# Optimization experiments

Measured on AMD Instinct MI355X. Metric: run time of the kernel, lower is better.

The kernel has to match this reference:

```python
import jax, jax.numpy as jnp
import numpy as np

LEVEL = 2
INV_SQRT2 = 0.7071067811865476
# subband order: index 0 is the approx (x_coeff1[0]); the 7 details match the
# {'aad','ada','add','daa','dad','dda','ddd'} dict keys of wavedec3 level-`LEVEL`.
SUBS = ['aaa', 'aad', 'ada', 'add', 'daa', 'dad', 'dda', 'ddd']


def dwt1(x, axis):
    # single-level Haar (db1, periodic) analysis along one axis
    x = jnp.moveaxis(x, axis, -1)
    n = x.shape[-1]
    x = x.reshape(*x.shape[:-1], n // 2, 2)
    a = (x[..., 0] + x[..., 1]) * INV_SQRT2
    d = (x[..., 0] - x[..., 1]) * INV_SQRT2
    return jnp.moveaxis(a, -1, axis), jnp.moveaxis(d, -1, axis)


def dwt3(x):
    # separable 3D Haar DWT over the last 3 axes -> 8 subbands keyed 'aaa'..'ddd'
    subs = {'': x}
    for axis in (-3, -2, -1):
        nxt = {}
        for k, v in subs.items():
            a, d = dwt1(v, axis)
            nxt[k + 'a'] = a
            nxt[k + 'd'] = d
        subs = nxt
    return subs


def idwt1(a, d, axis):
    a = jnp.moveaxis(a, axis, -1)
    d = jnp.moveaxis(d, axis, -1)
    x = jnp.stack([(a + d) * INV_SQRT2, (a - d) * INV_SQRT2], axis=-1)
    x = x.reshape(*x.shape[:-2], x.shape[-2] * 2)
    return jnp.moveaxis(x, -1, axis)


def idwt3(subs):
    for axis in (-1, -2, -3):
        prefixes = sorted(set(k[:-1] for k in subs))
        subs = {p: idwt1(subs[p + 'a'], subs[p + 'd'], axis) for p in prefixes}
    return subs['']


def upsample_zero_details(a):
    # one inverse-DWT level with all detail coeffs = 0 (finer levels are zeroed
    # in the original forward for jj in 2..level)
    for axis in (-3, -2, -1):
        a = jnp.repeat(a, 2, axis=axis) * INV_SQRT2
    return a


def setup_inputs() -> dict:
    key = jax.random.key(0)
    k1, k2, k3, k4 = jax.random.split(key, 4)
    B, C, D, H, W = 4, 32, 64, 64, 64
    m = D >> LEVEL  # 16 = modes1
    scale = 1.0 / (C * C)
    x_1 = jax.random.normal(k1, (B, C, D, H, W), dtype=jnp.float32)
    x_2 = jax.random.normal(k2, (B, C, D, H, W), dtype=jnp.float32)
    W1 = scale * jax.random.uniform(k3, (8, C, C, m, m, m), dtype=jnp.float32)
    W2 = scale * jax.random.uniform(k4, (8, C, C, m, m, m), dtype=jnp.float32)
    return {'x_1': x_1, 'x_2': x_2, 'W1': W1, 'W2': W2}


def reference(x_1, x_2, W1, W2):
    # batched wavelet decompose -> per-subband channel mixing of the coarsest
    # level (the only level the original transforms; finer details are zeroed)
    a1, a2 = x_1, x_2
    for _ in range(LEVEL):
        s1 = dwt3(a1)
        s2 = dwt3(a2)
        a1 = s1['aaa']
        a2 = s2['aaa']
    mixed = {}
    for idx, k in enumerate(SUBS):
        mixed[k] = (jnp.einsum('bixyz,ioxyz->boxyz', s1[k], W1[idx])
                    + jnp.einsum('bixyz,ioxyz->boxyz', s2[k], W2[idx]))
    x = idwt3(mixed)  # level LEVEL -> LEVEL-1
    for _ in range(LEVEL - 1):
        x = upsample_zero_details(x)
    return x
```

## Files before the change

### kernel.cpp

```cpp
#include <hip/hip_runtime.h>


#define M3 4096
#define KS 524288
#define IS 4194304

__global__ __launch_bounds__(256) void k_fwd(const float* __restrict__ x1,
                                             const float* __restrict__ x2,
                                             float* __restrict__ s) {
  const int tid = blockIdx.x * 256 + threadIdx.x;
  const int v  = tid & 4095;
  const int bc = tid >> 12;
  const int z = v & 15, y = (v >> 4) & 15, x = v >> 8;
  const size_t base = ((((size_t)bc * 64 + 4 * x) * 64 + 4 * y) * 64 + 4 * z);
  const float* __restrict__ p10 = x1 + base;
  const float* __restrict__ p11 = x1 + base + 2 * 4096;
  const float* __restrict__ p20 = x2 + base;
  const float* __restrict__ p21 = x2 + base + 2 * 4096;

  float4 a1[2][2], a2[2][2];
#pragma unroll
  for (int p = 0; p < 2; ++p)
#pragma unroll
    for (int q = 0; q < 2; ++q) {
      a1[p][q] = make_float4(0.f, 0.f, 0.f, 0.f);
      a2[p][q] = make_float4(0.f, 0.f, 0.f, 0.f);
    }

#pragma unroll
  for (int dp = 0; dp < 2; ++dp) {
#pragma unroll
    for (int hh = 0; hh < 4; ++hh) {
      const int off = (dp * 64 + hh) * 64;
      const float4 f10 = *reinterpret_cast<const float4*>(p10 + off);
      const float4 f20 = *reinterpret_cast<const float4*>(p20 + off);
      const float4 f11 = *reinterpret_cast<const float4*>(p11 + off);
      const float4 f21 = *reinterpret_cast<const float4*>(p21 + off);
      const int q = hh >> 1;
      a1[0][q].x += f10.x; a1[0][q].y += f10.y; a1[0][q].z += f10.z; a1[0][q].w += f10.w;
      a1[1][q].x += f11.x; a1[1][q].y += f11.y; a1[1][q].z += f11.z; a1[1][q].w += f11.w;
      a2[0][q].x += f20.x; a2[0][q].y += f20.y; a2[0][q].z += f20.z; a2[0][q].w += f20.w;
      a2[1][q].x += f21.x; a2[1][q].y += f21.y; a2[1][q].z += f21.z; a2[1][q].w += f21.w;
    }
  }

#pragma unroll
  for (int inp = 0; inp < 2; ++inp) {
    float4 (*A)[2] = inp ? a2 : a1;
    const float b0 = A[0][0].x + A[0][0].y, b1 = A[0][0].z + A[0][0].w;
    const float b2 = A[0][1].x + A[0][1].y, b3 = A[0][1].z + A[0][1].w;
    const float b4 = A[1][0].x + A[1][0].y, b5 = A[1][0].z + A[1][0].w;
    const float b6 = A[1][1].x + A[1][1].y, b7 = A[1][1].z + A[1][1].w;
    const float t0 = b0 + b1, t1 = b0 - b1, t2 = b2 + b3, t3 = b2 - b3;
    const float t4 = b4 + b5, t5 = b4 - b5, t6 = b6 + b7, t7 = b6 - b7;
    const float u0 = t0 + t2, u2 = t0 - t2, u1 = t1 + t3, u3 = t1 - t3;
    const float u4 = t4 + t6, u6 = t4 - t6, u5 = t5 + t7, u7 = t5 - t7;
    float* o = s + (size_t)inp * IS + (size_t)bc * M3 + v;
    o[0 * KS] = 0.125f * (u0 + u4);
    o[4 * KS] = 0.125f * (u0 - u4);
    o[1 * KS] = 0.125f * (u1 + u5);
    o[5 * KS] = 0.125f * (u1 - u5);
    o[2 * KS] = 0.125f * (u2 + u6);
    o[6 * KS] = 0.125f * (u2 - u6);
    o[3 * KS] = 0.125f * (u3 + u7);
    o[7 * KS] = 0.125f * (u3 - u7);
  }
}

__global__ __launch_bounds__(256) void k_mix(const float* __restrict__ W1,
                                             const float* __restrict__ W2,
                                             const float* __restrict__ s,
                                             float* __restrict__ mixed) {
  const int bid  = blockIdx.x;
  const int k    = bid & 7;
  const int rest = bid >> 3;
  const int og   = rest & 3;
  const int vblk = rest >> 2;
  const int v = vblk * 256 + threadIdx.x;
  const float* pW1 = W1 + ((size_t)k * 1024 + og * 8) * M3 + v;
  const float* pW2 = W2 + ((size_t)k * 1024 + og * 8) * M3 + v;
  const float* ps  = s + (size_t)k * KS + v;
  float acc[4][8];
#pragma unroll
  for (int b = 0; b < 4; ++b)
#pragma unroll
    for (int oo = 0; oo < 8; ++oo) acc[b][oo] = 0.f;
#pragma unroll 2
  for (int i = 0; i < 32; ++i) {
    float s1b[4], s2b[4];
#pragma unroll
    for (int b = 0; b < 4; ++b) {
      s1b[b] = ps[(size_t)(b * 32 + i) * M3];
      s2b[b] = ps[(size_t)IS + (size_t)(b * 32 + i) * M3];
    }
#pragma unroll
    for (int oo = 0; oo < 8; ++oo) {
      const float w1 = pW1[(size_t)(i * 32 + oo) * M3];
      const float w2 = pW2[(size_t)(i * 32 + oo) * M3];
#pragma unroll
      for (int b = 0; b < 4; ++b) acc[b][oo] += s1b[b] * w1 + s2b[b] * w2;
    }
  }
  float* pm = mixed + (size_t)k * KS + (size_t)og * 8 * M3 + v;
#pragma unroll
  for (int b = 0; b < 4; ++b)
#pragma unroll
    for (int oo = 0; oo < 8; ++oo)
      pm[(size_t)b * (32 * M3) + (size_t)oo * M3] = acc[b][oo];
}

__global__ __launch_bounds__(256) void k_inv(const float* __restrict__ mixed,
                                             float* __restrict__ out) {
  const int tid = blockIdx.x * 256 + threadIdx.x;
  const int v = tid & 4095;
  const int o = (tid >> 12) & 31;
  const int b = tid >> 17;
  const float* pm = mixed + (size_t)(b * 32 + o) * M3 + v;
  const float m0 = pm[0 * (size_t)KS], m1 = pm[1 * (size_t)KS];
  const float m2 = pm[2 * (size_t)KS], m3 = pm[3 * (size_t)KS];
  const float m4 = pm[4 * (size_t)KS], m5 = pm[5 * (size_t)KS];
  const float m6 = pm[6 * (size_t)KS], m7 = pm[7 * (size_t)KS];
  const float t0 = m0 + m1, t1 = m0 - m1, t2 = m2 + m3, t3 = m2 - m3;
  const float t4 = m4 + m5, t5 = m4 - m5, t6 = m6 + m7, t7 = m6 - m7;
  const float u0 = t0 + t2, u2 = t0 - t2, u1 = t1 + t3, u3 = t1 - t3;
  const float u4 = t4 + t6, u6 = t4 - t6, u5 = t5 + t7, u7 = t5 - t7;
  float w[2][2][2];
  w[0][0][0] = 0.125f * (u0 + u4);
  w[1][0][0] = 0.125f * (u0 - u4);
  w[0][0][1] = 0.125f * (u1 + u5);
  w[1][0][1] = 0.125f * (u1 - u5);
  w[0][1][0] = 0.125f * (u2 + u6);
  w[1][1][0] = 0.125f * (u2 - u6);
  w[0][1][1] = 0.125f * (u3 + u7);
  w[1][1][1] = 0.125f * (u3 - u7);
  const int z = v & 15, y = (v >> 4) & 15, x = v >> 8;
  float* base =
      out + ((((size_t)(b * 32 + o) * 64 + 4 * x) * 64 + 4 * y) * 64 + 4 * z);
#pragma unroll
  for (int dd = 0; dd < 4; ++dd) {
    const int p = dd >> 1;
#pragma unroll
    for (int hh = 0; hh < 4; ++hh) {
      const int q = hh >> 1;
      const float lo = w[p][q][0], hi = w[p][q][1];
      float4 f;
      f.x = lo; f.y = lo; f.z = hi; f.w = hi;
      *reinterpret_cast<float4*>(base + (dd * 64 + hh) * 64) = f;
    }
  }
}

extern "C" void kernel_launch(void* const* d_in, const int* in_sizes, int n_in,
                              void* d_out, int out_size, void* d_ws, size_t ws_size,
                              hipStream_t stream) {
  const float* x1 = (const float*)d_in[0];
  const float* x2 = (const float*)d_in[1];
  const float* W1 = (const float*)d_in[2];
  const float* W2 = (const float*)d_in[3];
  float* out = (float*)d_out;
  float* s     = (float*)d_ws;
  float* mixed = s + 2 * (size_t)IS;
  k_fwd<<<2048, 256, 0, stream>>>(x1, x2, s);
  k_mix<<<512, 256, 0, stream>>>(W1, W2, s, mixed);
  k_inv<<<2048, 256, 0, stream>>>(mixed, out);
}
```

Baseline: 166.5 us.

## Fuse channel mixing and inverse Haar upsampling into one kernel

Merges the mixing and inverse-transform kernels into one. Each block now owns a single output channel and 256 voxels, loops over all 8 subbands, and folds the inverse 8-point Haar butterfly in as sign-weighted accumulation before writing the upsampled output directly. This removes the intermediate `mixed` buffer write and read and one kernel launch. In exchange, each subband coefficient of `s` is reloaded once per output channel instead of being reused across 8 outputs, which raises cache traffic and load instruction count.

```diff
diff --git a/kernel.cpp b/kernel.cpp
--- a/kernel.cpp
+++ b/kernel.cpp
@@ -67,85 +67,64 @@
   }
 }
 
-__global__ __launch_bounds__(256) void k_mix(const float* __restrict__ W1,
-                                             const float* __restrict__ W2,
-                                             const float* __restrict__ s,
-                                             float* __restrict__ mixed) {
+__global__ __launch_bounds__(256) void k_mixinv(const float* __restrict__ W1,
+                                                const float* __restrict__ W2,
+                                                const float* __restrict__ s,
+                                                float* __restrict__ out) {
   const int bid  = blockIdx.x;
-  const int k    = bid & 7;
-  const int rest = bid >> 3;
-  const int og   = rest & 3;
-  const int vblk = rest >> 2;
+  const int vblk = bid & 15;
+  const int o    = bid >> 4;
   const int v = vblk * 256 + threadIdx.x;
-  const float* pW1 = W1 + ((size_t)k * 1024 + og * 8) * M3 + v;
-  const float* pW2 = W2 + ((size_t)k * 1024 + og * 8) * M3 + v;
-  const float* ps  = s + (size_t)k * KS + v;
+  const float* ps  = s + v;
+  const float* pW1 = W1 + (size_t)o * M3 + v;
+  const float* pW2 = W2 + (size_t)o * M3 + v;
+
   float acc[4][8];
 #pragma unroll
   for (int b = 0; b < 4; ++b)
 #pragma unroll
-    for (int oo = 0; oo < 8; ++oo) acc[b][oo] = 0.f;
+    for (int m = 0; m < 8; ++m) acc[b][m] = 0.f;
+
+  for (int k = 0; k < 8; ++k) {
+    const float* psk  = ps + (size_t)k * KS;
+    const float* pw1k = pW1 + (size_t)k * 1024 * M3;
+    const float* pw2k = pW2 + (size_t)k * 1024 * M3;
+    float mix[4] = {0.f, 0.f, 0.f, 0.f};
 #pragma unroll 2
-  for (int i = 0; i < 32; ++i) {
-    float s1b[4], s2b[4];
+    for (int i = 0; i < 32; ++i) {
+      const float w1 = pw1k[(size_t)(i * 32) * M3];
+      const float w2 = pw2k[(size_t)(i * 32) * M3];
 #pragma unroll
-    for (int b = 0; b < 4; ++b) {
-      s1b[b] = ps[(size_t)(b * 32 + i) * M3];
-      s2b[b] = ps[(size_t)IS + (size_t)(b * 32 + i) * M3];
+      for (int b = 0; b < 4; ++b) {
+        mix[b] += psk[(size_t)(b * 32 + i) * M3] * w1
+                + psk[(size_t)IS + (size_t)(b * 32 + i) * M3] * w2;
+      }
     }
 #pragma unroll
-    for (int oo = 0; oo < 8; ++oo) {
-      const float w1 = pW1[(size_t)(i * 32 + oo) * M3];
-      const float w2 = pW2[(size_t)(i * 32 + oo) * M3];
+    for (int m = 0; m < 8; ++m) {
+      const float sgn = (__popc(k & m) & 1) ? -1.f : 1.f;
 #pragma unroll
-      for (int b = 0; b < 4; ++b) acc[b][oo] += s1b[b] * w1 + s2b[b] * w2;
+      for (int b = 0; b < 4; ++b) acc[b][m] += sgn * mix[b];
     }
   }
-  float* pm = mixed + (size_t)k * KS + (size_t)og * 8 * M3 + v;
+
+  const int z = v & 15, y = (v >> 4) & 15, x = v >> 8;
 #pragma unroll
-  for (int b = 0; b < 4; ++b)
+  for (int b = 0; b < 4; ++b) {
+    float* base =
+        out + ((((size_t)(b * 32 + o) * 64 + 4 * x) * 64 + 4 * y) * 64 + 4 * z);
 #pragma unroll
-    for (int oo = 0; oo < 8; ++oo)
-      pm[(size_t)b * (32 * M3) + (size_t)oo * M3] = acc[b][oo];
-}
-
-__global__ __launch_bounds__(256) void k_inv(const float* __restrict__ mixed,
-                                             float* __restrict__ out) {
-  const int tid = blockIdx.x * 256 + threadIdx.x;
-  const int v = tid & 4095;
-  const int o = (tid >> 12) & 31;
-  const int b = tid >> 17;
-  const float* pm = mixed + (size_t)(b * 32 + o) * M3 + v;
-  const float m0 = pm[0 * (size_t)KS], m1 = pm[1 * (size_t)KS];
-  const float m2 = pm[2 * (size_t)KS], m3 = pm[3 * (size_t)KS];
-  const float m4 = pm[4 * (size_t)KS], m5 = pm[5 * (size_t)KS];
-  const float m6 = pm[6 * (size_t)KS], m7 = pm[7 * (size_t)KS];
-  const float t0 = m0 + m1, t1 = m0 - m1, t2 = m2 + m3, t3 = m2 - m3;
-  const float t4 = m4 + m5, t5 = m4 - m5, t6 = m6 + m7, t7 = m6 - m7;
-  const float u0 = t0 + t2, u2 = t0 - t2, u1 = t1 + t3, u3 = t1 - t3;
-  const float u4 = t4 + t6, u6 = t4 - t6, u5 = t5 + t7, u7 = t5 - t7;
-  float w[2][2][2];
-  w[0][0][0] = 0.125f * (u0 + u4);
-  w[1][0][0] = 0.125f * (u0 - u4);
-  w[0][0][1] = 0.125f * (u1 + u5);
-  w[1][0][1] = 0.125f * (u1 - u5);
-  w[0][1][0] = 0.125f * (u2 + u6);
-  w[1][1][0] = 0.125f * (u2 - u6);
-  w[0][1][1] = 0.125f * (u3 + u7);
-  w[1][1][1] = 0.125f * (u3 - u7);
-  const int z = v & 15, y = (v >> 4) & 15, x = v >> 8;
-  float* base =
-      out + ((((size_t)(b * 32 + o) * 64 + 4 * x) * 64 + 4 * y) * 64 + 4 * z);
+    for (int dd = 0; dd < 4; ++dd) {
+      const int p = dd >> 1;
 #pragma unroll
-  for (int dd = 0; dd < 4; ++dd) {
-    const int p = dd >> 1;
-#pragma unroll
-    for (int hh = 0; hh < 4; ++hh) {
-      const int q = hh >> 1;
-      const float lo = w[p][q][0], hi = w[p][q][1];
-      float4 f;
-      f.x = lo; f.y = lo; f.z = hi; f.w = hi;
-      *reinterpret_cast<float4*>(base + (dd * 64 + hh) * 64) = f;
+      for (int hh = 0; hh < 4; ++hh) {
+        const int q = hh >> 1;
+        const float lo = 0.125f * acc[b][p * 4 + q * 2 + 0];
+        const float hi = 0.125f * acc[b][p * 4 + q * 2 + 1];
+        float4 f;
+        f.x = lo; f.y = lo; f.z = hi; f.w = hi;
+        *reinterpret_cast<float4*>(base + (dd * 64 + hh) * 64) = f;
+      }
     }
   }
 }
@@ -158,9 +137,7 @@
   const float* W1 = (const float*)d_in[2];
   const float* W2 = (const float*)d_in[3];
   float* out = (float*)d_out;
-  float* s     = (float*)d_ws;
-  float* mixed = s + 2 * (size_t)IS;
+  float* s = (float*)d_ws;
   k_fwd<<<2048, 256, 0, stream>>>(x1, x2, s);
-  k_mix<<<512, 256, 0, stream>>>(W1, W2, s, mixed);
-  k_inv<<<2048, 256, 0, stream>>>(mixed, out);
+  k_mixinv<<<512, 256, 0, stream>>>(W1, W2, s, out);
 }
```

Result: slower. 211.0 us (+26.7%).
